# Kernel optimization log

Measured on AMD Instinct MI355X. Metric: run time of the kernel, lower is better.

## Reference

```python
import jax, jax.numpy as jnp
import numpy as np

N_NODES = 100000
N_EDGES = 1600000
N_GRAPHS = 512
F_IN = 20
HID = 128
OUT = HID // 2


def _glorot(key, shape):
    fan_in, fan_out = shape[0], shape[1]
    lim = float(np.sqrt(6.0 / (fan_in + fan_out)))
    return jax.random.uniform(key, shape, jnp.float32, -lim, lim)


def setup_inputs() -> dict:
    key = jax.random.key(0)
    ks = jax.random.split(key, 12)
    x = jax.random.normal(ks[0], (N_NODES, F_IN), jnp.float32)
    edge_index = jax.random.randint(ks[1], (2, N_EDGES), 0, N_NODES, dtype=jnp.int64)
    batch = jnp.sort(jax.random.randint(ks[2], (N_NODES,), 0, N_GRAPHS, dtype=jnp.int64))
    return {
        "x": x,
        "edge_index": edge_index,
        "batch": batch,
        "W1": _glorot(ks[3], (F_IN, HID)), "b1": jnp.zeros((HID,), jnp.float32),
        "W2": _glorot(ks[4], (HID, HID)), "b2": jnp.zeros((HID,), jnp.float32),
        "W3": _glorot(ks[5], (HID, HID)), "b3": jnp.zeros((HID,), jnp.float32),
        "Wout": _glorot(ks[6], (HID, OUT)), "bout": jnp.zeros((OUT,), jnp.float32),
    }


def _gcn_conv(x, W, b, src, dst, num_nodes):
    # PyG GCNConv: x' = D^{-1/2} (A + I) D^{-1/2} X W + b (self-loops already in src/dst)
    xw = x @ W                                                  # [N, H]
    ones = jnp.ones(src.shape[0], dtype=xw.dtype)
    deg = jax.ops.segment_sum(ones, dst, num_segments=num_nodes)
    dinv = jnp.where(deg > 0, jax.lax.rsqrt(deg), 0.0)          # [N]
    norm = dinv[src] * dinv[dst]                                # [E+N]
    msg = xw[src] * norm[:, None]                               # gather + scale
    return jax.ops.segment_sum(msg, dst, num_segments=num_nodes) + b


def reference(x, edge_index, batch, W1, b1, W2, b2, W3, b3, Wout, bout):
    num_nodes = x.shape[0]
    loops = jnp.arange(num_nodes, dtype=edge_index.dtype)
    src = jnp.concatenate([edge_index[0], loops])
    dst = jnp.concatenate([edge_index[1], loops])

    h = jax.nn.relu(_gcn_conv(x, W1, b1, src, dst, num_nodes))
    h = jax.nn.relu(_gcn_conv(h, W2, b2, src, dst, num_nodes))
    h = jax.nn.relu(_gcn_conv(h, W3, b3, src, dst, num_nodes))

    # global_mean_pool over graph ids
    sums = jax.ops.segment_sum(h, batch, num_segments=N_GRAPHS)
    counts = jax.ops.segment_sum(jnp.ones(num_nodes, h.dtype), batch, num_segments=N_GRAPHS)
    pooled = sums / jnp.maximum(counts, 1.0)[:, None]           # [G, H]
    return pooled @ Wout + bout                                 # [G, H//2]
```

## Files before the change

kernel.cpp:

```cpp
#include <hip/hip_runtime.h>
#include <hip/hip_fp16.h>

#define N_NODES 100000
#define N_EDGES 1600000
#define N_GRAPHS 512
#define F_IN 20
#define HID 128
#define OUT_F 64

#define BUCKETS 512
#define SPAN 196
#define BCAP 3500
#define EPB 4096

typedef _Float16 half8_t __attribute__((ext_vector_type(8)));
typedef float f32x4_t __attribute__((ext_vector_type(4)));

__device__ inline float4 h4_to_f4(uint2 u) {
    __half2 h0 = *(__half2*)&u.x;
    __half2 h1 = *(__half2*)&u.y;
    float2 f0 = __half22float2(h0);
    float2 f1 = __half22float2(h1);
    return make_float4(f0.x, f0.y, f1.x, f1.y);
}

__global__ __launch_bounds__(512) void partition(const int* __restrict__ src,
                                                 const int* __restrict__ dst,
                                                 int* __restrict__ bpairs,
                                                 int* cur512) {
    __shared__ int lcnt[8][BUCKETS];
    __shared__ int woff[8][BUCKETS];
    int t = threadIdx.x;
    int wv = t >> 6;
    for (int i = t; i < 8 * BUCKETS; i += 512) ((int*)lcnt)[i] = 0;
    __syncthreads();
    int base = blockIdx.x * EPB;
    int myb[8], myp[8], myr[8];
#pragma unroll
    for (int i = 0; i < 8; ++i) {
        int e = base + i * 512 + t;
        int b = -1, p = 0, rk = 0;
        if (e < N_EDGES) {
            int s = src[e], d = dst[e];
            b = d / SPAN;
            p = (s << 9) | (d - b * SPAN);
            rk = atomicAdd(&lcnt[wv][b], 1);
        }
        myb[i] = b; myp[i] = p; myr[i] = rk;
    }
    __syncthreads();
    {
        int c[8], tot = 0;
#pragma unroll
        for (int w = 0; w < 8; ++w) { c[w] = lcnt[w][t]; tot += c[w]; }
        int gb = atomicAdd(&cur512[t], tot);
#pragma unroll
        for (int w = 0; w < 8; ++w) { woff[w][t] = gb; gb += c[w]; }
    }
    __syncthreads();
#pragma unroll
    for (int i = 0; i < 8; ++i) {
        int b = myb[i];
        if (b >= 0) {
            int p = woff[wv][b] + myr[i];
            if (p < BCAP) bpairs[(size_t)b * BCAP + p] = myp[i];
        }
    }
}

__global__ __launch_bounds__(512) void csr_build(const int* __restrict__ bpairs,
                                                 const int* __restrict__ cur512,
                                                 int* __restrict__ row_st,
                                                 int* __restrict__ csr,
                                                 const float* __restrict__ x,
                                                 __half* __restrict__ Xs) {
    __shared__ int ocnt[SPAN];
    __shared__ int cur[SPAN];
    __shared__ int wtot[8];
    __shared__ int sbase_s;
    int b = blockIdx.x, t = threadIdx.x;
    int lane = t & 63, w = t >> 6;

    int n0 = b * SPAN;
    int span = N_NODES - n0; if (span > SPAN) span = SPAN;
    if (span < 0) span = 0;
    if (t < SPAN) ocnt[t] = 0;

    int myc = cur512[t];
    int inc = myc;
#pragma unroll
    for (int off = 1; off < 64; off <<= 1) {
        int v = __shfl_up(inc, off);
        if (lane >= off) inc += v;
    }
    if (lane == 63) wtot[w] = inc;
    __syncthreads();
    {
        int wbase = 0;
#pragma unroll
        for (int j = 0; j < 8; ++j) wbase += (j < w) ? wtot[j] : 0;
        int ex = wbase + inc - myc;
        if (t == b) sbase_s = ex;
    }
    if (b == BUCKETS - 1 && t == 0) row_st[N_NODES] = N_EDGES;

    int n = cur512[b];
    if (n > BCAP) n = BCAP;
    const int* p = bpairs + (size_t)b * BCAP;
    for (int i = t; i < n; i += 512) atomicAdd(&ocnt[p[i] & 511], 1);
    __syncthreads();

    int v2 = (t < span) ? ocnt[t] : 0;
    int inc2 = v2;
#pragma unroll
    for (int off = 1; off < 64; off <<= 1) {
        int v = __shfl_up(inc2, off);
        if (lane >= off) inc2 += v;
    }
    if (lane == 63) wtot[w] = inc2;
    __syncthreads();
    {
        int wbase = 0;
#pragma unroll
        for (int j = 0; j < 8; ++j) wbase += (j < w) ? wtot[j] : 0;
        int start = wbase + inc2 - v2;
        if (t < span) {
            row_st[n0 + t] = sbase_s + start;
            cur[t] = start;
        }
    }
    __syncthreads();

    int base = sbase_s;
    for (int i = t; i < n; i += 512) {
        int e = p[i];
        int lp = atomicAdd(&cur[e & 511], 1);
        csr[base + lp] = e >> 9;
    }
    for (int i = t; i < span * 32; i += 512) {
        int nl = i >> 5, f = i & 31;
        float v = (f < F_IN) ? x[(size_t)(n0 + nl) * F_IN + f] : 0.f;
        float di = rsqrtf((float)(ocnt[nl] + 1));
        Xs[(size_t)(n0 + nl) * 32 + f] = __float2half(di * v);
    }
}

__global__ __launch_bounds__(256) void layer1(const __half* __restrict__ Xs,
                                              const int* __restrict__ row_st,
                                              const int* __restrict__ csr,
                                              const float* __restrict__ W,
                                              const float* __restrict__ bias,
                                              __half* __restrict__ H) {
    __shared__ float Wlds[F_IN * HID];
    const int t = threadIdx.x;
    const int node0 = blockIdx.x * 16;
    for (int i = t; i < F_IN * HID; i += 256) Wlds[i] = W[i];
    __syncthreads();

    const int grp = t >> 4;
    const int l16 = t & 15;
    const int gbase = t & 48;
    const __half2* X2 = (const __half2*)Xs;

    int nn = node0 + grp;
    int r0 = row_st[nn], r1 = row_st[nn + 1];
    float2 acc = __half22float2(X2[(size_t)nn * 16 + l16]);
    int r = r0;
    for (; r + 3 < r1; r += 4) {
        float2 f0 = __half22float2(X2[(size_t)csr[r] * 16 + l16]);
        float2 f1 = __half22float2(X2[(size_t)csr[r + 1] * 16 + l16]);
        float2 f2 = __half22float2(X2[(size_t)csr[r + 2] * 16 + l16]);
        float2 f3 = __half22float2(X2[(size_t)csr[r + 3] * 16 + l16]);
        acc.x += (f0.x + f1.x) + (f2.x + f3.x);
        acc.y += (f0.y + f1.y) + (f2.y + f3.y);
    }
    for (; r < r1; ++r) {
        float2 f = __half22float2(X2[(size_t)csr[r] * 16 + l16]);
        acc.x += f.x; acc.y += f.y;
    }
    float di = rsqrtf((float)(r1 - r0 + 1));
    acc.x *= di; acc.y *= di;

    const int c0 = l16 * 8;
    float4 oa = *(const float4*)&bias[c0];
    float4 ob = *(const float4*)&bias[c0 + 4];
#pragma unroll
    for (int k = 0; k < F_IN; ++k) {
        float a = __shfl((k & 1) ? acc.y : acc.x, gbase + (k >> 1), 64);
        float4 w0 = *(const float4*)&Wlds[k * HID + c0];
        float4 w1 = *(const float4*)&Wlds[k * HID + c0 + 4];
        oa.x = fmaf(a, w0.x, oa.x); oa.y = fmaf(a, w0.y, oa.y);
        oa.z = fmaf(a, w0.z, oa.z); oa.w = fmaf(a, w0.w, oa.w);
        ob.x = fmaf(a, w1.x, ob.x); ob.y = fmaf(a, w1.y, ob.y);
        ob.z = fmaf(a, w1.z, ob.z); ob.w = fmaf(a, w1.w, ob.w);
    }
    __half2 h0 = __floats2half2_rn(oa.x, oa.y);
    __half2 h1 = __floats2half2_rn(oa.z, oa.w);
    __half2 h2 = __floats2half2_rn(ob.x, ob.y);
    __half2 h3 = __floats2half2_rn(ob.z, ob.w);
    uint4 u;
    u.x = *(unsigned*)&h0; u.y = *(unsigned*)&h1;
    u.z = *(unsigned*)&h2; u.w = *(unsigned*)&h3;
    ((uint4*)H)[(size_t)nn * 16 + l16] = u;
}

__global__ __launch_bounds__(256) void gemm_mfma(const __half* __restrict__ H,
                                                 const float* __restrict__ W,
                                                 const int* __restrict__ row_st,
                                                 __half* __restrict__ T) {
    __shared__ _Float16 Whi[64 * 128];
    __shared__ _Float16 Wlo[64 * 128];
    const int t = threadIdx.x;
    const int c0 = (blockIdx.x & 1) * 64;

    for (int i = t; i < 128 * 64; i += 256) {
        int k = i >> 6, c = i & 63;
        float w = W[k * HID + c0 + c];
        _Float16 hi = (_Float16)w;
        _Float16 lo = (_Float16)((w - (float)hi) * 2048.0f);
        int addr = c * 128 + (((k >> 3) ^ (c & 15)) << 3) + (k & 7);
        Whi[addr] = hi;
        Wlo[addr] = lo;
    }
    __syncthreads();

    const int wv = t >> 6;
    const int l  = t & 63;
    const int lr = l & 15;
    const int lq = l >> 4;

    for (int rep = 0; rep < 4; ++rep) {
        int strip = ((blockIdx.x >> 1) * 4 + wv) * 4 + rep;
        if (strip >= N_NODES / 16) continue;
        int n0 = strip * 16;

        f32x4_t acc[4], acl[4];
#pragma unroll
        for (int ct = 0; ct < 4; ++ct) { acc[ct] = (f32x4_t){0,0,0,0}; acl[ct] = (f32x4_t){0,0,0,0}; }

#pragma unroll
        for (int kc = 0; kc < 4; ++kc) {
            half8_t a = *(const half8_t*)(H + (size_t)(n0 + lr) * 128 + kc * 32 + lq * 8);
#pragma unroll
            for (int j = 0; j < 8; ++j) a[j] = a[j] > (_Float16)0 ? a[j] : (_Float16)0;
            int g = kc * 4 + lq;
#pragma unroll
            for (int ct = 0; ct < 4; ++ct) {
                int c = ct * 16 + lr;
                int addr = c * 128 + ((g ^ lr) << 3);
                half8_t bh = *(const half8_t*)&Whi[addr];
                half8_t bl = *(const half8_t*)&Wlo[addr];
                acc[ct] = __builtin_amdgcn_mfma_f32_16x16x32_f16(a, bh, acc[ct], 0, 0, 0);
                acl[ct] = __builtin_amdgcn_mfma_f32_16x16x32_f16(a, bl, acl[ct], 0, 0, 0);
            }
        }

        int r0 = n0 + lq * 4;
#pragma unroll
        for (int r = 0; r < 4; ++r) {
            int row = r0 + r;
            float d = rsqrtf((float)(row_st[row + 1] - row_st[row] + 1));
#pragma unroll
            for (int ct = 0; ct < 4; ++ct) {
                float v = (acc[ct][r] + acl[ct][r] * 4.8828125e-4f) * d;
                T[(size_t)row * 128 + c0 + ct * 16 + lr] = __float2half(v);
            }
        }
    }
}

__global__ __launch_bounds__(256) void gather_range(const __half* __restrict__ A,
                                                    const int* __restrict__ row_st,
                                                    const int* __restrict__ csr,
                                                    const float* __restrict__ bias,
                                                    __half* __restrict__ B) {
    int t = threadIdx.x;
    int n = blockIdx.x * 8 + (t >> 5);
    int l = t & 31;
    int r0 = row_st[n], r1 = row_st[n + 1];
    float di = rsqrtf((float)(r1 - r0 + 1));
    const uint2* Af = (const uint2*)A;
    float4 acc = h4_to_f4(Af[n * 32 + l]);
    int r = r0;
    for (; r + 7 < r1; r += 8) {
        int s0 = csr[r],     s1 = csr[r + 1], s2 = csr[r + 2], s3 = csr[r + 3];
        int s4 = csr[r + 4], s5 = csr[r + 5], s6 = csr[r + 6], s7 = csr[r + 7];
        float4 v0 = h4_to_f4(Af[s0 * 32 + l]);
        float4 v1 = h4_to_f4(Af[s1 * 32 + l]);
        float4 v2 = h4_to_f4(Af[s2 * 32 + l]);
        float4 v3 = h4_to_f4(Af[s3 * 32 + l]);
        float4 v4 = h4_to_f4(Af[s4 * 32 + l]);
        float4 v5 = h4_to_f4(Af[s5 * 32 + l]);
        float4 v6 = h4_to_f4(Af[s6 * 32 + l]);
        float4 v7 = h4_to_f4(Af[s7 * 32 + l]);
        acc.x += ((v0.x + v1.x) + (v2.x + v3.x)) + ((v4.x + v5.x) + (v6.x + v7.x));
        acc.y += ((v0.y + v1.y) + (v2.y + v3.y)) + ((v4.y + v5.y) + (v6.y + v7.y));
        acc.z += ((v0.z + v1.z) + (v2.z + v3.z)) + ((v4.z + v5.z) + (v6.z + v7.z));
        acc.w += ((v0.w + v1.w) + (v2.w + v3.w)) + ((v4.w + v5.w) + (v6.w + v7.w));
    }
    for (; r + 3 < r1; r += 4) {
        int s0 = csr[r], s1 = csr[r + 1], s2 = csr[r + 2], s3 = csr[r + 3];
        float4 v0 = h4_to_f4(Af[s0 * 32 + l]);
        float4 v1 = h4_to_f4(Af[s1 * 32 + l]);
        float4 v2 = h4_to_f4(Af[s2 * 32 + l]);
        float4 v3 = h4_to_f4(Af[s3 * 32 + l]);
        acc.x += (v0.x + v1.x) + (v2.x + v3.x);
        acc.y += (v0.y + v1.y) + (v2.y + v3.y);
        acc.z += (v0.z + v1.z) + (v2.z + v3.z);
        acc.w += (v0.w + v1.w) + (v2.w + v3.w);
    }
    for (; r < r1; ++r) {
        float4 v = h4_to_f4(Af[csr[r] * 32 + l]);
        acc.x += v.x; acc.y += v.y; acc.z += v.z; acc.w += v.w;
    }
    float4 b4 = ((const float4*)bias)[l];
    __half2 h0 = __floats2half2_rn(fmaf(di, acc.x, b4.x), fmaf(di, acc.y, b4.y));
    __half2 h1 = __floats2half2_rn(fmaf(di, acc.z, b4.z), fmaf(di, acc.w, b4.w));
    uint2 u; u.x = *(unsigned*)&h0; u.y = *(unsigned*)&h1;
    ((uint2*)B)[n * 32 + l] = u;
}

__global__ __launch_bounds__(256) void pool_head(const __half* __restrict__ H,
                                                 const int* __restrict__ batch,
                                                 const float* __restrict__ Wout,
                                                 const float* __restrict__ bout,
                                                 float* __restrict__ out) {
    __shared__ float4 part[8][32];
    __shared__ float p[HID];
    __shared__ int bounds[2];
    int g = blockIdx.x;
    int t = threadIdx.x;
    if (t < 2) {
        int target = g + t;
        int lo = 0, hi = N_NODES;
        while (lo < hi) {
            int mid = (lo + hi) >> 1;
            if (batch[mid] < target) lo = mid + 1; else hi = mid;
        }
        bounds[t] = lo;
    }
    __syncthreads();
    int lo = bounds[0], hi = bounds[1];
    int grp = t >> 5, l = t & 31;
    const uint2* Hf = (const uint2*)H;
    float4 acc = make_float4(0.f, 0.f, 0.f, 0.f);
    for (int n = lo + grp; n < hi; n += 8) {
        float4 v = h4_to_f4(Hf[(size_t)n * 32 + l]);
        acc.x += fmaxf(v.x, 0.f);
        acc.y += fmaxf(v.y, 0.f);
        acc.z += fmaxf(v.z, 0.f);
        acc.w += fmaxf(v.w, 0.f);
    }
    part[grp][l] = acc;
    __syncthreads();
    if (t < 32) {
        float4 s = part[0][t];
#pragma unroll
        for (int j = 1; j < 8; ++j) {
            float4 v = part[j][t];
            s.x += v.x; s.y += v.y; s.z += v.z; s.w += v.w;
        }
        float inv = 1.0f / fmaxf((float)(hi - lo), 1.0f);
        p[t * 4 + 0] = s.x * inv;
        p[t * 4 + 1] = s.y * inv;
        p[t * 4 + 2] = s.z * inv;
        p[t * 4 + 3] = s.w * inv;
    }
    __syncthreads();
    if (t < OUT_F) {
        float acc2 = 0.f;
#pragma unroll 8
        for (int k = 0; k < HID; ++k)
            acc2 = fmaf(p[k], Wout[k * OUT_F + t], acc2);
        out[g * OUT_F + t] = acc2 + bout[t];
    }
}

extern "C" void kernel_launch(void* const* d_in, const int* in_sizes, int n_in,
                              void* d_out, int out_size, void* d_ws, size_t ws_size,
                              hipStream_t stream) {
    const float* x     = (const float*)d_in[0];
    const int*   ei    = (const int*)d_in[1];
    const int*   batch = (const int*)d_in[2];
    const float* W1    = (const float*)d_in[3];
    const float* b1    = (const float*)d_in[4];
    const float* W2    = (const float*)d_in[5];
    const float* b2    = (const float*)d_in[6];
    const float* W3    = (const float*)d_in[7];
    const float* b3    = (const float*)d_in[8];
    const float* Wout  = (const float*)d_in[9];
    const float* bout  = (const float*)d_in[10];
    float* out = (float*)d_out;

    const int* src = ei;
    const int* dst = ei + N_EDGES;

    float* A      = (float*)d_ws;
    float* Breg   = A + (size_t)N_NODES * HID;
    int*   row_st = (int*)(Breg + (size_t)N_NODES * HID);
    int*   cur512 = row_st + N_NODES + 1;
    int*   csr    = cur512 + BUCKETS;

    int*    bpairs = (int*)A;
    __half* Xs     = (__half*)((char*)A + 7168000);
    __half* T      = (__half*)A;
    __half* H      = (__half*)Breg;

    hipMemsetAsync(cur512, 0, BUCKETS * sizeof(int), stream);
    partition<<<(N_EDGES + EPB - 1) / EPB, 512, 0, stream>>>(src, dst, bpairs, cur512);
    csr_build<<<BUCKETS, 512, 0, stream>>>(bpairs, cur512, row_st, csr, x, Xs);

    layer1<<<N_NODES / 16, 256, 0, stream>>>(Xs, row_st, csr, W1, b1, H);

    gemm_mfma<<<782, 256, 0, stream>>>(H, W2, row_st, T);
    gather_range<<<N_NODES / 8, 256, 0, stream>>>(T, row_st, csr, b2, H);
    gemm_mfma<<<782, 256, 0, stream>>>(H, W3, row_st, T);
    gather_range<<<N_NODES / 8, 256, 0, stream>>>(T, row_st, csr, b3, H);

    pool_head<<<N_GRAPHS, 256, 0, stream>>>(H, batch, Wout, bout, out);
}
```

Before: 356.0 us.

## Store node features in column-sliced slabs so gather works per 16-channel slice

```diff
diff --git a/kernel.cpp b/kernel.cpp
--- a/kernel.cpp
+++ b/kernel.cpp
@@ -12,6 +12,8 @@
 #define SPAN 196
 #define BCAP 3500
 #define EPB 4096
+
+#define SLAB ((size_t)N_NODES * 16)
 
 typedef _Float16 half8_t __attribute__((ext_vector_type(8)));
 typedef float f32x4_t __attribute__((ext_vector_type(4)));
@@ -201,7 +203,7 @@
     uint4 u;
     u.x = *(unsigned*)&h0; u.y = *(unsigned*)&h1;
     u.z = *(unsigned*)&h2; u.w = *(unsigned*)&h3;
-    ((uint4*)H)[(size_t)nn * 16 + l16] = u;
+    *(uint4*)(H + (size_t)(l16 >> 1) * SLAB + (size_t)nn * 16 + (l16 & 1) * 8) = u;
 }
 
 __global__ __launch_bounds__(256) void gemm_mfma(const __half* __restrict__ H,
@@ -240,7 +242,9 @@
 
 #pragma unroll
         for (int kc = 0; kc < 4; ++kc) {
-            half8_t a = *(const half8_t*)(H + (size_t)(n0 + lr) * 128 + kc * 32 + lq * 8);
+            int coff = kc * 32 + lq * 8;
+            half8_t a = *(const half8_t*)(H + (size_t)(coff >> 4) * SLAB
+                                            + (size_t)(n0 + lr) * 16 + (coff & 15));
 #pragma unroll
             for (int j = 0; j < 8; ++j) a[j] = a[j] > (_Float16)0 ? a[j] : (_Float16)0;
             int g = kc * 4 + lq;
@@ -263,36 +267,38 @@
 #pragma unroll
             for (int ct = 0; ct < 4; ++ct) {
                 float v = (acc[ct][r] + acl[ct][r] * 4.8828125e-4f) * d;
-                T[(size_t)row * 128 + c0 + ct * 16 + lr] = __float2half(v);
+                T[(size_t)((c0 >> 4) + ct) * SLAB + (size_t)row * 16 + lr] = __float2half(v);
             }
         }
     }
 }
 
-__global__ __launch_bounds__(256) void gather_range(const __half* __restrict__ A,
+__global__ __launch_bounds__(256) void gather_slice(const __half* __restrict__ T,
                                                     const int* __restrict__ row_st,
                                                     const int* __restrict__ csr,
                                                     const float* __restrict__ bias,
-                                                    __half* __restrict__ B) {
+                                                    __half* __restrict__ H) {
     int t = threadIdx.x;
-    int n = blockIdx.x * 8 + (t >> 5);
-    int l = t & 31;
+    int s = blockIdx.x & 7;
+    int n = (blockIdx.x >> 3) * 64 + (t >> 2);
+    int l = t & 3;
+    if (n >= N_NODES) return;
+    const uint2* Tf = (const uint2*)(T + (size_t)s * SLAB);
     int r0 = row_st[n], r1 = row_st[n + 1];
     float di = rsqrtf((float)(r1 - r0 + 1));
-    const uint2* Af = (const uint2*)A;
-    float4 acc = h4_to_f4(Af[n * 32 + l]);
+    float4 acc = h4_to_f4(Tf[(size_t)n * 4 + l]);
     int r = r0;
     for (; r + 7 < r1; r += 8) {
         int s0 = csr[r],     s1 = csr[r + 1], s2 = csr[r + 2], s3 = csr[r + 3];
         int s4 = csr[r + 4], s5 = csr[r + 5], s6 = csr[r + 6], s7 = csr[r + 7];
-        float4 v0 = h4_to_f4(Af[s0 * 32 + l]);
-        float4 v1 = h4_to_f4(Af[s1 * 32 + l]);
-        float4 v2 = h4_to_f4(Af[s2 * 32 + l]);
-        float4 v3 = h4_to_f4(Af[s3 * 32 + l]);
-        float4 v4 = h4_to_f4(Af[s4 * 32 + l]);
-        float4 v5 = h4_to_f4(Af[s5 * 32 + l]);
-        float4 v6 = h4_to_f4(Af[s6 * 32 + l]);
-        float4 v7 = h4_to_f4(Af[s7 * 32 + l]);
+        float4 v0 = h4_to_f4(Tf[(size_t)s0 * 4 + l]);
+        float4 v1 = h4_to_f4(Tf[(size_t)s1 * 4 + l]);
+        float4 v2 = h4_to_f4(Tf[(size_t)s2 * 4 + l]);
+        float4 v3 = h4_to_f4(Tf[(size_t)s3 * 4 + l]);
+        float4 v4 = h4_to_f4(Tf[(size_t)s4 * 4 + l]);
+        float4 v5 = h4_to_f4(Tf[(size_t)s5 * 4 + l]);
+        float4 v6 = h4_to_f4(Tf[(size_t)s6 * 4 + l]);
+        float4 v7 = h4_to_f4(Tf[(size_t)s7 * 4 + l]);
         acc.x += ((v0.x + v1.x) + (v2.x + v3.x)) + ((v4.x + v5.x) + (v6.x + v7.x));
         acc.y += ((v0.y + v1.y) + (v2.y + v3.y)) + ((v4.y + v5.y) + (v6.y + v7.y));
         acc.z += ((v0.z + v1.z) + (v2.z + v3.z)) + ((v4.z + v5.z) + (v6.z + v7.z));
@@ -300,24 +306,24 @@
     }
     for (; r + 3 < r1; r += 4) {
         int s0 = csr[r], s1 = csr[r + 1], s2 = csr[r + 2], s3 = csr[r + 3];
-        float4 v0 = h4_to_f4(Af[s0 * 32 + l]);
-        float4 v1 = h4_to_f4(Af[s1 * 32 + l]);
-        float4 v2 = h4_to_f4(Af[s2 * 32 + l]);
-        float4 v3 = h4_to_f4(Af[s3 * 32 + l]);
+        float4 v0 = h4_to_f4(Tf[(size_t)s0 * 4 + l]);
+        float4 v1 = h4_to_f4(Tf[(size_t)s1 * 4 + l]);
+        float4 v2 = h4_to_f4(Tf[(size_t)s2 * 4 + l]);
+        float4 v3 = h4_to_f4(Tf[(size_t)s3 * 4 + l]);
         acc.x += (v0.x + v1.x) + (v2.x + v3.x);
         acc.y += (v0.y + v1.y) + (v2.y + v3.y);
         acc.z += (v0.z + v1.z) + (v2.z + v3.z);
         acc.w += (v0.w + v1.w) + (v2.w + v3.w);
     }
     for (; r < r1; ++r) {
-        float4 v = h4_to_f4(Af[csr[r] * 32 + l]);
+        float4 v = h4_to_f4(Tf[(size_t)csr[r] * 4 + l]);
         acc.x += v.x; acc.y += v.y; acc.z += v.z; acc.w += v.w;
     }
-    float4 b4 = ((const float4*)bias)[l];
+    float4 b4 = *(const float4*)&bias[s * 16 + l * 4];
     __half2 h0 = __floats2half2_rn(fmaf(di, acc.x, b4.x), fmaf(di, acc.y, b4.y));
     __half2 h1 = __floats2half2_rn(fmaf(di, acc.z, b4.z), fmaf(di, acc.w, b4.w));
     uint2 u; u.x = *(unsigned*)&h0; u.y = *(unsigned*)&h1;
-    ((uint2*)B)[n * 32 + l] = u;
+    ((uint2*)(H + (size_t)s * SLAB))[(size_t)n * 4 + l] = u;
 }
 
 __global__ __launch_bounds__(256) void pool_head(const __half* __restrict__ H,
@@ -342,10 +348,10 @@
     __syncthreads();
     int lo = bounds[0], hi = bounds[1];
     int grp = t >> 5, l = t & 31;
-    const uint2* Hf = (const uint2*)H;
+    const __half* Hs = H + (size_t)(l >> 2) * SLAB + (size_t)(l & 3) * 4;
     float4 acc = make_float4(0.f, 0.f, 0.f, 0.f);
     for (int n = lo + grp; n < hi; n += 8) {
-        float4 v = h4_to_f4(Hf[(size_t)n * 32 + l]);
+        float4 v = h4_to_f4(*(const uint2*)(Hs + (size_t)n * 16));
         acc.x += fmaxf(v.x, 0.f);
         acc.y += fmaxf(v.y, 0.f);
         acc.z += fmaxf(v.z, 0.f);
@@ -412,10 +418,11 @@
 
     layer1<<<N_NODES / 16, 256, 0, stream>>>(Xs, row_st, csr, W1, b1, H);
 
+    const int gat_grid = ((N_NODES + 63) / 64) * 8;
     gemm_mfma<<<782, 256, 0, stream>>>(H, W2, row_st, T);
-    gather_range<<<N_NODES / 8, 256, 0, stream>>>(T, row_st, csr, b2, H);
+    gather_slice<<<gat_grid, 256, 0, stream>>>(T, row_st, csr, b2, H);
     gemm_mfma<<<782, 256, 0, stream>>>(H, W3, row_st, T);
-    gather_range<<<N_NODES / 8, 256, 0, stream>>>(T, row_st, csr, b3, H);
+    gather_slice<<<gat_grid, 256, 0, stream>>>(T, row_st, csr, b3, H);
 
     pool_head<<<N_GRAPHS, 256, 0, stream>>>(H, batch, Wout, bout, out);
 }
```

New measurement: 392.9 us. +10.4%, slower.
